# Kernel tuning notes

Measured on AMD Instinct MI355X. Metric: run time of the kernel, lower is better.

## Reference

```python
import jax, jax.numpy as jnp
import numpy as np

B, S, D, C, K, V = 128, 512, 300, 300, 3, 30000  # batch, seq, embed=hidden, capsule, categories, vocab
PAD_INDEX = 0
SQUASH_EPS = 1e-8
MASK_NEG = -1e9


def squash(x, axis=-1):
    # v * (|v|^2 / (1+|v|^2)) / |v|
    sq = jnp.sum(x * x, axis=axis, keepdims=True)
    return (sq / (1.0 + sq)) * x / jnp.sqrt(sq + SQUASH_EPS)


def setup_inputs() -> dict:
    key = jax.random.key(0)
    ks = jax.random.split(key, 11)
    return {
        "sentence": jax.random.randint(ks[0], (B, S), 0, V),
        "aspect": jax.random.randint(ks[1], (B,), 0, V),
        "category_alpha": jax.random.uniform(ks[2], (B, S), dtype=jnp.float32),
        "embed": jax.random.normal(ks[3], (V, D), dtype=jnp.float32) * 0.02,
        "W_s": jax.random.normal(ks[4], (D, C), dtype=jnp.float32) * 0.02,
        "b_s": jnp.zeros((C,), dtype=jnp.float32),
        "W_a": jax.random.normal(ks[5], (D, C), dtype=jnp.float32) * 0.02,
        "b_a": jnp.zeros((C,), dtype=jnp.float32),
        "W_att": jax.random.normal(ks[6], (C, C), dtype=jnp.float32) * 0.02,
        "guide_capsule": jax.random.normal(ks[7], (K, C), dtype=jnp.float32) * 0.02,
        "guide_weight": jax.random.normal(ks[8], (C, C), dtype=jnp.float32) * 0.02,
        "scale": jnp.asarray(5.0, dtype=jnp.float32),
    }


def reference(sentence, aspect, category_alpha, embed, W_s, b_s, W_a, b_a,
              W_att, guide_capsule, guide_weight, scale):
    mask = sentence != PAD_INDEX                      # [B,S]
    emb = embed[sentence]                             # [B,S,D]
    asp = embed[aspect]                               # [B,D]

    # element_wise_mul (vectorized): per-token alpha weighting
    caml = emb * category_alpha[..., None]            # [B,S,D]
    cavl = jnp.sum(caml, axis=1)                      # [B,D] (unused in non-Cav path)
    del cavl

    # _sentence_encode stand-in (abstract in source): alpha-weighted embeddings
    sent_enc = caml                                   # [B,S,hidden=D]

    primary = squash(sent_enc @ W_s + b_s)            # [B,S,C]
    aspect_capsule = squash(asp @ W_a + b_a)          # [B,C]

    # bilinear attention weights with padding mask, softmax over sequence
    scores = jnp.einsum('bsc,cd,bd->bs', primary, W_att, aspect_capsule)
    scores = jnp.where(mask, scores, MASK_NEG)
    norm_weight = jax.nn.softmax(scores, axis=-1)     # [B,S]

    # capsule-guided routing
    guide = squash(guide_capsule)                     # [K,C]
    gm = jnp.einsum('bsc,cd,kd->bsk', primary, guide_weight, guide)
    gm = jax.nn.softmax(gm, axis=-1) * norm_weight[..., None] * scale
    category_capsule = squash(jnp.einsum('bsk,bsc->bkc', gm, primary))  # [B,K,C]

    return jnp.sqrt(jnp.sum(category_capsule * category_capsule, axis=-1))  # [B,K]
```

## Files before the change

### kernel.cpp

```cpp
#include <hip/hip_runtime.h>

#define NV 30000
#define NB 128
#define NS 512
#define ND 300
#define NC 300
#define CP 304
#define KP 320
#define MASK_NEG -1e9f
#define SQ_EPS 1e-8f

typedef __attribute__((ext_vector_type(4))) float f32x4;
typedef __attribute__((ext_vector_type(8))) __bf16 bf16x8;

__device__ __forceinline__ unsigned int f2bfu(float x){
  unsigned int u = __float_as_uint(x);
  u += 0x7FFFu + ((u >> 16) & 1u);
  return u >> 16;
}
__device__ __forceinline__ unsigned short f2bf(float x){ return (unsigned short)f2bfu(x); }

__device__ __forceinline__ int swzk(int row, int k){
  return (k & ~0x38) | (((((k >> 3) & 7) ^ (row & 7)) & 7) << 3);
}

__device__ __forceinline__ float bsum512(float v, float* red, int tid){
  red[tid] = v; __syncthreads();
  float s = 0.f;
  if (tid < 64){
    s = red[tid]+red[tid+64]+red[tid+128]+red[tid+192]
      + red[tid+256]+red[tid+320]+red[tid+384]+red[tid+448];
    #pragma unroll
    for (int off = 32; off > 0; off >>= 1) s += __shfl_xor(s, off);
    if (tid == 0) red[0] = s;
  }
  __syncthreads();
  s = red[0];
  __syncthreads();
  return s;
}

__device__ __forceinline__ float bmax512(float v, float* red, int tid){
  red[tid] = v; __syncthreads();
  float s = MASK_NEG;
  if (tid < 64){
    s = red[tid];
    #pragma unroll
    for (int o = 64; o < 512; o += 64) s = fmaxf(s, red[tid+o]);
    #pragma unroll
    for (int off = 32; off > 0; off >>= 1) s = fmaxf(s, __shfl_xor(s, off));
    if (tid == 0) red[0] = s;
  }
  __syncthreads();
  s = red[0];
  __syncthreads();
  return s;
}

__global__ __launch_bounds__(512) void kA(
    const float* __restrict__ Ws, const float* __restrict__ Wa,
    const float* __restrict__ ba, const int* __restrict__ aspect,
    const float* __restrict__ embed, const float* __restrict__ gcap,
    const float* __restrict__ Gw, const float* __restrict__ bs,
    unsigned short* __restrict__ WTC, float* __restrict__ ZG,
    float* __restrict__ Z2P, float* __restrict__ TG)
{
  __shared__ __align__(16) char shm[55296];
  int bid = blockIdx.x, tid = threadIdx.x;
  int lane = tid & 63, wid = tid >> 6;
  if (bid < 25){
    float (*t)[65] = (float(*)[65])shm;
    int kt = bid / 5, nt = bid - kt*5;
    #pragma unroll
    for (int i = 0; i < 8; i++){
      int idx = i*512 + tid;
      int r = idx >> 6, c = idx & 63;
      int gk = kt*64 + r, gn = nt*64 + c;
      t[r][c] = (gk < ND && gn < NC) ? Ws[gk*NC + gn] : 0.f;
    }
    __syncthreads();
    #pragma unroll
    for (int i = 0; i < 8; i++){
      int idx = i*512 + tid;
      int n = idx >> 6, k = idx & 63;
      int row = nt*64 + n, gk = kt*64 + k;
      WTC[(size_t)row*KP + swzk(row, gk)] = f2bf(t[k][n]);
    }
    if (bid < 24){
      for (int r = 0; r < 8; r++){
        int row = 320 + bid*8 + r;
        if (tid < KP) WTC[(size_t)row*KP + tid] = 0;
      }
    }
  } else if (bid < 45){
    unsigned short (*ATF)[72] = (unsigned short (*)[72])shm;
    unsigned short (*ldbz)[72] = (unsigned short (*)[72])(shm + 128*144);
    int* toksh = (int*)(shm + 144*144);
    int zb = bid - 25;
    int nc0 = zb * 16;
    if (tid < 128) toksh[tid] = aspect[tid];
    __syncthreads();
    f32x4 accz = {0.f,0.f,0.f,0.f};
    for (int s = 0; s < 5; s++){
      int k0 = s*64;
      #pragma unroll
      for (int i = 0; i < 4; i++){
        int idx = i*512 + tid;
        int row = idx >> 4, q = idx & 15;
        int gk = k0 + 4*q;
        float4 v = {0.f,0.f,0.f,0.f};
        if (gk < ND) v = *(const float4*)(embed + (size_t)toksh[row]*ND + gk);
        uint2 pk; pk.x = f2bfu(v.x)|(f2bfu(v.y)<<16); pk.y = f2bfu(v.z)|(f2bfu(v.w)<<16);
        *(uint2*)(&ATF[row][4*q]) = pk;
      }
      if (tid < 256){
        int dl = tid >> 2, qq = tid & 3;
        int d = k0 + dl, c = nc0 + 4*qq;
        float4 v = {0.f,0.f,0.f,0.f};
        if (d < ND && c < NC) v = *(const float4*)(Wa + (size_t)d*NC + c);
        ldbz[4*qq+0][dl] = f2bf(v.x);
        ldbz[4*qq+1][dl] = f2bf(v.y);
        ldbz[4*qq+2][dl] = f2bf(v.z);
        ldbz[4*qq+3][dl] = f2bf(v.w);
      }
      __syncthreads();
      #pragma unroll
      for (int kk = 0; kk < 64; kk += 32){
        int kl = kk + (lane >> 4)*8;
        bf16x8 a = *(const bf16x8*)(&ATF[wid*16 + (lane & 15)][kl]);
        bf16x8 b = *(const bf16x8*)(&ldbz[lane & 15][kl]);
        accz = __builtin_amdgcn_mfma_f32_16x16x32_bf16(a, b, accz, 0, 0, 0);
      }
      __syncthreads();
    }
    int zc = nc0 + (lane & 15);
    float bav = (zc < NC) ? ba[zc] : 0.f;
    #pragma unroll
    for (int j = 0; j < 4; j++){
      int row = wid*16 + ((lane >> 4) << 2) + j;
      float zv = (zc < NC) ? (accz[j] + bav) : 0.f;
      ZG[(size_t)row*KP + zc] = zv;
      float p = zv*zv;
      #pragma unroll
      for (int off = 1; off < 16; off <<= 1) p += __shfl_xor(p, off);
      if ((lane & 15) == 0) Z2P[zb*128 + row] = p;
    }
  } else {
    unsigned short (*Ag)[328] = (unsigned short (*)[328])shm;
    unsigned short (*ldbg)[328] = (unsigned short (*)[328])(shm + 16*656);
    float* red = (float*)(shm + 80*656);
    int gb = bid - 45, c0 = gb*64;
    for (int k = 0; k < 3; k++){
      float g = (tid < NC) ? gcap[k*NC + tid] : 0.f;
      float sq = bsum512(g*g, red, tid);
      float ssv = (sq/(1.f+sq))/sqrtf(sq + SQ_EPS);
      if (tid < 328) Ag[k][tid] = (tid < NC) ? f2bf(g*ssv) : (unsigned short)0;
    }
    for (int r = 3; r < 16; r++) if (tid < 328) Ag[r][tid] = 0;
    #pragma unroll
    for (int i = 0; i < 10; i++){
      int idx = i*512 + tid;
      int cl = idx / 80, q = idx - cl*80;
      float4 v = {0.f,0.f,0.f,0.f};
      if (c0 + cl < NC && q < 75) v = *(const float4*)(Gw + (size_t)(c0+cl)*NC + 4*q);
      uint2 pk; pk.x = f2bfu(v.x)|(f2bfu(v.y)<<16); pk.y = f2bfu(v.z)|(f2bfu(v.w)<<16);
      *(uint2*)(&ldbg[cl][4*q]) = pk;
    }
    __syncthreads();
    if (wid < 4){
      f32x4 acc = {0.f,0.f,0.f,0.f};
      #pragma unroll
      for (int kk = 0; kk < KP; kk += 32){
        int kidx = kk + (lane >> 4)*8;
        bf16x8 a = *(const bf16x8*)(&Ag[lane & 15][kidx]);
        bf16x8 b = *(const bf16x8*)(&ldbg[wid*16 + (lane & 15)][kidx]);
        acc = __builtin_amdgcn_mfma_f32_16x16x32_bf16(a, b, acc, 0, 0, 0);
      }
      #pragma unroll
      for (int j = 0; j < 4; j++){
        int r = ((lane >> 4) << 2) + j;
        if (r < 3) TG[(size_t)(128 + r)*KP + c0 + wid*16 + (lane & 15)] = acc[j];
      }
    }
    if (gb == 0 && tid < KP) TG[(size_t)131*KP + tid] = (tid < NC) ? bs[tid] : 0.f;
  }
}

__global__ __launch_bounds__(512) void kB(
    const float* __restrict__ ZG, const float* __restrict__ Z2P,
    const float* __restrict__ Watt, float* __restrict__ TG)
{
  __shared__ unsigned short ATF[128][72];
  __shared__ unsigned short ldbt[16][72];
  __shared__ float ssb[128];
  int tid = threadIdx.x, lane = tid & 63, wid = tid >> 6;
  int c0 = blockIdx.x * 16;
  if (tid < 128){
    float s = 0.f;
    #pragma unroll
    for (int i = 0; i < 20; i++) s += Z2P[i*128 + tid];
    ssb[tid] = (s/(1.f+s))/sqrtf(s + SQ_EPS);
  }
  __syncthreads();
  f32x4 acct = {0.f,0.f,0.f,0.f};
  for (int s = 0; s < 5; s++){
    int k0 = s*64;
    #pragma unroll
    for (int i = 0; i < 4; i++){
      int idx = i*512 + tid;
      int row = idx >> 4, q = idx & 15;
      float4 v = *(const float4*)(ZG + (size_t)row*KP + k0 + 4*q);
      float sv = ssb[row];
      uint2 pk; pk.x = f2bfu(v.x*sv)|(f2bfu(v.y*sv)<<16); pk.y = f2bfu(v.z*sv)|(f2bfu(v.w*sv)<<16);
      *(uint2*)(&ATF[row][4*q]) = pk;
    }
    if (tid < 256){
      int cl = tid >> 4, q = tid & 15;
      int gc = k0 + 4*q;
      float4 v = {0.f,0.f,0.f,0.f};
      if (c0 + cl < NC && gc < NC) v = *(const float4*)(Watt + (size_t)(c0+cl)*NC + gc);
      uint2 pk; pk.x = f2bfu(v.x)|(f2bfu(v.y)<<16); pk.y = f2bfu(v.z)|(f2bfu(v.w)<<16);
      *(uint2*)(&ldbt[cl][4*q]) = pk;
    }
    __syncthreads();
    #pragma unroll
    for (int kk = 0; kk < 64; kk += 32){
      int kl = kk + (lane >> 4)*8;
      bf16x8 a = *(const bf16x8*)(&ATF[wid*16 + (lane & 15)][kl]);
      bf16x8 b = *(const bf16x8*)(&ldbt[lane & 15][kl]);
      acct = __builtin_amdgcn_mfma_f32_16x16x32_bf16(a, b, acct, 0, 0, 0);
    }
    __syncthreads();
  }
  int cc = c0 + (lane & 15);
  #pragma unroll
  for (int j = 0; j < 4; j++){
    int row = wid*16 + ((lane >> 4) << 2) + j;
    TG[(size_t)row*KP + cc] = acct[j];
  }
}

__global__ __launch_bounds__(512) void kC(
    const float* __restrict__ TG, const float* __restrict__ Ws,
    const float* __restrict__ bs,
    unsigned short* __restrict__ WTC, float* __restrict__ BC)
{
  __shared__ unsigned short ATF[144][72];
  __shared__ unsigned short ldbw[16][72];
  int tid = threadIdx.x, lane = tid & 63, wid = tid >> 6;
  int wb = blockIdx.x;
  int d0 = wb*16;
  f32x4 aw0 = {0.f,0.f,0.f,0.f}, aw8 = {0.f,0.f,0.f,0.f};
  for (int s = 0; s < 5; s++){
    int k0 = s*64;
    #pragma unroll
    for (int i = 0; i < 5; i++){
      int idx = i*512 + tid;
      if (idx < 2304){
        int row = idx >> 4, q = idx & 15;
        float4 v = {0.f,0.f,0.f,0.f};
        if (row < 132) v = *(const float4*)(TG + (size_t)row*KP + k0 + 4*q);
        uint2 pk; pk.x = f2bfu(v.x)|(f2bfu(v.y)<<16); pk.y = f2bfu(v.z)|(f2bfu(v.w)<<16);
        *(uint2*)(&ATF[row][4*q]) = pk;
      }
    }
    if (tid < 256){
      int dl = tid >> 4, q = tid & 15;
      int gc = k0 + 4*q;
      float4 v = {0.f,0.f,0.f,0.f};
      if (gc < NC){
        if (wb < 20){ if (d0 + dl < ND) v = *(const float4*)(Ws + (size_t)(d0+dl)*NC + gc); }
        else if (dl == 0) v = *(const float4*)(bs + gc);
      }
      uint2 pk; pk.x = f2bfu(v.x)|(f2bfu(v.y)<<16); pk.y = f2bfu(v.z)|(f2bfu(v.w)<<16);
      *(uint2*)(&ldbw[dl][4*q]) = pk;
    }
    __syncthreads();
    #pragma unroll
    for (int kk = 0; kk < 64; kk += 32){
      int kl = kk + (lane >> 4)*8;
      bf16x8 b = *(const bf16x8*)(&ldbw[lane & 15][kl]);
      bf16x8 a = *(const bf16x8*)(&ATF[wid*16 + (lane & 15)][kl]);
      aw0 = __builtin_amdgcn_mfma_f32_16x16x32_bf16(a, b, aw0, 0, 0, 0);
      bf16x8 a8 = *(const bf16x8*)(&ATF[128 + (lane & 15)][kl]);
      aw8 = __builtin_amdgcn_mfma_f32_16x16x32_bf16(a8, b, aw8, 0, 0, 0);
    }
    __syncthreads();
  }
  int gd = lane & 15;
  #pragma unroll
  for (int j = 0; j < 4; j++){
    int row = wid*16 + ((lane >> 4) << 2) + j;
    if (wb < 20){
      int col = d0 + gd;
      if (col < ND) WTC[(size_t)(320 + row)*KP + swzk(320 + row, col)] = f2bf(aw0[j]);
    } else if (gd == 0) BC[row] = aw0[j];
    if (wid == 0){
      int row8 = 128 + ((lane >> 4) << 2) + j;
      if (row8 < 132){
        if (wb < 20){
          int col = d0 + gd;
          if (col < ND) WTC[(size_t)(320 + row8)*KP + swzk(320 + row8, col)] = f2bf(aw8[j]);
        } else if (gd == 0) BC[row8] = aw8[j];
      }
    }
  }
}

#define LDK 72
__global__ __launch_bounds__(512, 4) void k1f(
    const float* __restrict__ embed, const unsigned short* __restrict__ WTC,
    float* __restrict__ EtT, float* __restrict__ ETS)
{
  __shared__ unsigned short lds_a[64*LDK];
  __shared__ unsigned short lds_b[512*64];
  __shared__ float e2part[3][64];
  int tid = threadIdx.x, lane = tid & 63, wid = tid >> 6;
  int wrow = wid >> 2, wcol = wid & 3;
  int rowbase = blockIdx.x * 64;
  f32x4 acc[2][8];
  f32x4 zero = {0.f,0.f,0.f,0.f};
  #pragma unroll
  for (int m = 0; m < 2; m++)
    #pragma unroll
    for (int n = 0; n < 8; n++) acc[m][n] = zero;

  float4 pa[2];
  auto loadA = [&](int k0){
    #pragma unroll
    for (int r = 0; r < 2; r++){
      int id = r*512 + tid;
      int row = id >> 4, k4 = (id & 15) << 2;
      int grow = rowbase + row, gk = k0 + k4;
      float4 v = {0.f,0.f,0.f,0.f};
      if (grow < NV && gk < ND) v = *(const float4*)(embed + (size_t)grow*ND + gk);
      pa[r] = v;
    }
  };
  auto writeA = [&](){
    #pragma unroll
    for (int r = 0; r < 2; r++){
      int id = r*512 + tid;
      int row = id >> 4, k4 = (id & 15) << 2;
      uint2 pk;
      pk.x = f2bfu(pa[r].x) | (f2bfu(pa[r].y) << 16);
      pk.y = f2bfu(pa[r].z) | (f2bfu(pa[r].w) << 16);
      *(uint2*)(lds_a + row*LDK + k4) = pk;
    }
  };
  auto stageB = [&](int k0){
    #pragma unroll
    for (int r = 0; r < 8; r++){
      int id = r*512 + tid;
      const unsigned short* gsrc = WTC + (size_t)(id >> 3)*KP + k0 + (id & 7)*8;
      __builtin_amdgcn_global_load_lds(
        (const __attribute__((address_space(1))) unsigned int*)gsrc,
        (__attribute__((address_space(3))) unsigned int*)((char*)lds_b + id*16),
        16, 0, 0);
    }
  };

  loadA(0);
  writeA();
  stageB(0);
  loadA(64);
  __syncthreads();
  for (int step = 0; step < 5; step++){
    #pragma unroll
    for (int kk = 0; kk < 64; kk += 32){
      int kidx = kk + (lane >> 4)*8;
      bf16x8 af[2];
      #pragma unroll
      for (int m = 0; m < 2; m++)
        af[m] = *(const bf16x8*)(lds_a + (wrow*32 + (lane & 15) + m*16)*LDK + kidx);
      #pragma unroll
      for (int n = 0; n < 8; n++){
        int jrow = wcol*128 + n*16 + (lane & 15);
        int ch = ((kidx >> 3) & 7) ^ (jrow & 7);
        bf16x8 bv = *(const bf16x8*)((const char*)lds_b + jrow*128 + ch*16);
        #pragma unroll
        for (int m = 0; m < 2; m++)
          acc[m][n] = __builtin_amdgcn_mfma_f32_16x16x32_bf16(af[m], bv, acc[m][n], 0, 0, 0);
      }
    }
    __syncthreads();
    if (step < 4){
      stageB((step+1)*64);
      writeA();
      if (step < 3) loadA((step+2)*64);
      __syncthreads();
    }
  }

  float* etile = (float*)lds_b;
  float* stile = (float*)((char*)lds_b + 32768);
  int rloc = wrow*32 + ((lane >> 4) << 2);
  #pragma unroll
  for (int m = 0; m < 2; m++)
    #pragma unroll
    for (int n = 0; n < 8; n++){
      int col = wcol*128 + n*16 + (lane & 15);
      #pragma unroll
      for (int j = 0; j < 4; j++){
        int rl = rloc + m*16 + j;
        if (col >= 320 && col < 448)      etile[rl*128 + (col - 320)] = acc[m][n][j];
        else if (col >= 448 && col < 452) stile[rl*8 + (col - 448)] = acc[m][n][j];
      }
    }
  #pragma unroll
  for (int m = 0; m < 2; m++)
    #pragma unroll
    for (int j = 0; j < 4; j++){
      float p = 0.f;
      #pragma unroll
      for (int n = 0; n < 8; n++)
        if (wcol*128 + n*16 < 320){ float t = acc[m][n][j]; p += t*t; }
      #pragma unroll
      for (int off = 1; off < 16; off <<= 1) p += __shfl_xor(p, off);
      if ((lane & 15) == 0 && wcol < 3) e2part[wcol][rloc + m*16 + j] = p;
    }
  __syncthreads();
  if (tid < 64){
    stile[tid*8 + 4] = e2part[0][tid] + e2part[1][tid] + e2part[2][tid];
    stile[tid*8 + 5] = 0.f; stile[tid*8 + 6] = 0.f; stile[tid*8 + 7] = 0.f;
  }
  __syncthreads();
  int nrow = NV - rowbase; if (nrow > 64) nrow = 64;
  float4* edst = (float4*)(EtT + (size_t)rowbase*128);
  const float4* esrc = (const float4*)etile;
  int e4 = nrow*32;
  for (int i = tid; i < e4; i += 512) edst[i] = esrc[i];
  float4* sdst = (float4*)(ETS + (size_t)rowbase*8);
  const float4* ssrc = (const float4*)stile;
  int s4 = nrow*2;
  for (int i = tid; i < s4; i += 512) sdst[i] = ssrc[i];
}

__global__ __launch_bounds__(512) void k45a(
    const int* __restrict__ sentence, const float* __restrict__ alpha,
    const float* __restrict__ scale_p, const float* __restrict__ embed,
    const float* __restrict__ EtT, const float* __restrict__ ETS,
    const float* __restrict__ BC, float* __restrict__ SBB, float* __restrict__ PRT)
{
  int bid = blockIdx.x;
  int b = bid >> 1, hb = bid & 1;
  int tid = threadIdx.x, lane = tid & 63, w = tid >> 6;
  __shared__ float red[512];
  __shared__ float cfs[NS*3];
  __shared__ int toksh[NS];
  __shared__ float cap8[8][3][CP];

  int idx = (b << 9) + tid;
  int tok = sentence[idx];
  float al = alpha[idx];
  toksh[tid] = tok;
  float et = EtT[(size_t)tok*128 + b];
  float4 eg = *(const float4*)(ETS + (size_t)tok*8);
  float e2 = ETS[(size_t)tok*8 + 4];
  float bst = BC[b];
  float bsg0 = BC[128], bsg1 = BC[129], bsg2 = BC[130], bs2 = BC[131];

  float sq = al*al*e2 + 2.f*al*eg.w + bs2;
  float ssv = (sq/(1.f+sq))/sqrtf(sq + SQ_EPS);
  float scv = (tok != 0) ? ssv*(al*et + bst) : MASK_NEG;
  float u0 = ssv*(al*eg.x + bsg0);
  float u1 = ssv*(al*eg.y + bsg1);
  float u2 = ssv*(al*eg.z + bsg2);

  float m = bmax512(scv, red, tid);
  float e = expf(scv - m);
  float Z = bsum512(e, red, tid);
  float nw = e / Z;
  float mk = fmaxf(u0, fmaxf(u1, u2));
  float e0 = expf(u0-mk), e1 = expf(u1-mk), e2k = expf(u2-mk);
  float wf = nw * scale_p[0] / (e0+e1+e2k);
  float w0 = e0*wf, w1 = e1*wf, w2 = e2k*wf;
  float ca = ssv * al;
  cfs[tid*3+0] = w0*ca; cfs[tid*3+1] = w1*ca; cfs[tid*3+2] = w2*ca;
  float sb0 = bsum512(w0*ssv, red, tid);
  float sb1 = bsum512(w1*ssv, red, tid);
  float sb2 = bsum512(w2*ssv, red, tid);
  if (hb == 0 && tid == 0){ SBB[b*3+0] = sb0; SBB[b*3+1] = sb1; SBB[b*3+2] = sb2; }
  __syncthreads();

  f32x4 A0 = {0.f,0.f,0.f,0.f}, A1 = A0, A2 = A0, R0 = A0, R1 = A0, R2 = A0;
  int c0 = lane << 2;
  int c1 = 256 + (lane << 2);
  bool rem = lane < 11;
  int base = (hb << 8) + (w << 5);
  #pragma unroll 4
  for (int i = 0; i < 32; i++){
    int s = base + i;
    int t = toksh[s];
    const float* er = embed + (size_t)t*ND;
    float4 y = *(const float4*)(er + c0);
    float cf0 = cfs[s*3+0], cf1 = cfs[s*3+1], cf2 = cfs[s*3+2];
    f32x4 yv = {y.x, y.y, y.z, y.w};
    A0 += cf0*yv; A1 += cf1*yv; A2 += cf2*yv;
    if (rem){
      float4 y2 = *(const float4*)(er + c1);
      f32x4 y2v = {y2.x, y2.y, y2.z, y2.w};
      R0 += cf0*y2v; R1 += cf1*y2v; R2 += cf2*y2v;
    }
  }
  *(f32x4*)&cap8[w][0][c0] = A0;
  *(f32x4*)&cap8[w][1][c0] = A1;
  *(f32x4*)&cap8[w][2][c0] = A2;
  if (rem){
    *(f32x4*)&cap8[w][0][c1] = R0;
    *(f32x4*)&cap8[w][1][c1] = R1;
    *(f32x4*)&cap8[w][2][c1] = R2;
  }
  __syncthreads();
  for (int p = tid; p < 3*CP; p += 512){
    int k = p / CP, c = p - k*CP;
    float v = 0.f;
    if (c < 300){
      #pragma unroll
      for (int w8 = 0; w8 < 8; w8++) v += cap8[w8][k][c];
    }
    PRT[((size_t)bid*3 + k)*CP + c] = v;
  }
}

__global__ __launch_bounds__(512) void k45b(
    const float* __restrict__ PRT, const float* __restrict__ SBB,
    const float* __restrict__ bs, const float* __restrict__ Ws,
    float* __restrict__ out)
{
  int b = blockIdx.x, tid = threadIdx.x;
  __shared__ float Qs[3][CP];
  __shared__ float red[512];
  for (int p = tid; p < 3*CP; p += 512){
    int k = p / CP, c = p - k*CP;
    float v = 0.f;
    if (c < 300)
      v = PRT[((size_t)(2*b)*3 + k)*CP + c] + PRT[((size_t)(2*b+1)*3 + k)*CP + c];
    Qs[k][c] = v;
  }
  __syncthreads();
  float v0 = 0.f, v1 = 0.f, v2 = 0.f;
  if (tid < NC){
    float a0=0.f,a1=0.f,a2=0.f,b0=0.f,b1=0.f,b2=0.f;
    for (int d = 0; d < 300; d += 2){
      float wA = Ws[d*NC + tid], wB = Ws[(d+1)*NC + tid];
      a0 += wA*Qs[0][d]; b0 += wB*Qs[0][d+1];
      a1 += wA*Qs[1][d]; b1 += wB*Qs[1][d+1];
      a2 += wA*Qs[2][d]; b2 += wB*Qs[2][d+1];
    }
    float bc = bs[tid];
    v0 = a0+b0 + SBB[b*3+0]*bc;
    v1 = a1+b1 + SBB[b*3+1]*bc;
    v2 = a2+b2 + SBB[b*3+2]*bc;
  }
  float s0 = bsum512(v0*v0, red, tid);
  float s1 = bsum512(v1*v1, red, tid);
  float s2 = bsum512(v2*v2, red, tid);
  if (tid == 0){
    out[b*3+0] = (s0/(1.f+s0))*sqrtf(s0)/sqrtf(s0 + SQ_EPS);
    out[b*3+1] = (s1/(1.f+s1))*sqrtf(s1)/sqrtf(s1 + SQ_EPS);
    out[b*3+2] = (s2/(1.f+s2))*sqrtf(s2)/sqrtf(s2 + SQ_EPS);
  }
}

extern "C" void kernel_launch(void* const* d_in, const int* in_sizes, int n_in,
                              void* d_out, int out_size, void* d_ws, size_t ws_size,
                              hipStream_t stream)
{
  (void)in_sizes; (void)n_in; (void)out_size; (void)ws_size;
  const int*   sentence = (const int*)d_in[0];
  const int*   aspect   = (const int*)d_in[1];
  const float* alpha    = (const float*)d_in[2];
  const float* embed    = (const float*)d_in[3];
  const float* Ws       = (const float*)d_in[4];
  const float* bs       = (const float*)d_in[5];
  const float* Wa       = (const float*)d_in[6];
  const float* ba       = (const float*)d_in[7];
  const float* Watt     = (const float*)d_in[8];
  const float* gcap     = (const float*)d_in[9];
  const float* gw       = (const float*)d_in[10];
  const float* scale    = (const float*)d_in[11];
  float* out = (float*)d_out;

  char* w = (char*)d_ws;
  auto alloc = [&](size_t bytes)->char*{
    char* p = w; w += (bytes + 255) & ~(size_t)255; return p;
  };
  unsigned short* WTC = (unsigned short*)alloc((size_t)512*KP*2);
  float* ZG  = (float*)alloc((size_t)128*KP*4);
  float* Z2P = (float*)alloc((size_t)20*128*4);
  float* TG  = (float*)alloc((size_t)132*KP*4);
  float* BC  = (float*)alloc(136*4);
  float* ETT = (float*)alloc((size_t)NV*128*4);
  float* ETS = (float*)alloc((size_t)NV*8*4);
  float* SBB = (float*)alloc(NB*3*4);
  float* PRT = (float*)alloc((size_t)256*3*CP*4);

  kA<<<50, 512, 0, stream>>>(Ws, Wa, ba, aspect, embed, gcap, gw, bs, WTC, ZG, Z2P, TG);
  kB<<<20, 512, 0, stream>>>(ZG, Z2P, Watt, TG);
  kC<<<21, 512, 0, stream>>>(TG, Ws, bs, WTC, BC);
  k1f<<<(NV + 63)/64, 512, 0, stream>>>(embed, WTC, ETT, ETS);
  k45a<<<256, 512, 0, stream>>>(sentence, alpha, scale, embed, ETT, ETS, BC, SBB, PRT);
  k45b<<<NB, 512, 0, stream>>>(PRT, SBB, bs, Ws, out);
}
```

Baseline: 93.27 us.

## Fuse kB and kC into one kernel, recomputing the full TG tile per block

Merges the two small GEMM kernels kB and kC into a single kernel, kBC. Each of the 21 blocks now computes the entire 128x300 TG product from Watt into LDS instead of reading it back from global memory. This removes one kernel launch and the global round-trip of TG between launches. The cost is redundant compute in every block, a large LDS footprint that can limit occupancy, and 19 accumulator vectors per thread that raise register pressure.

```diff
diff --git a/kernel.cpp b/kernel.cpp
--- a/kernel.cpp
+++ b/kernel.cpp
@@ -186,15 +186,20 @@
   }
 }
 
-__global__ __launch_bounds__(512) void kB(
+__global__ __launch_bounds__(512) void kBC(
     const float* __restrict__ ZG, const float* __restrict__ Z2P,
-    const float* __restrict__ Watt, float* __restrict__ TG)
+    const float* __restrict__ Watt, const float* __restrict__ TG,
+    const float* __restrict__ Ws, const float* __restrict__ bs,
+    unsigned short* __restrict__ WTC, float* __restrict__ BC)
 {
+  __shared__ unsigned short TL[144][328];
   __shared__ unsigned short ATF[128][72];
-  __shared__ unsigned short ldbt[16][72];
+  __shared__ unsigned short LB[304][72];
   __shared__ float ssb[128];
   int tid = threadIdx.x, lane = tid & 63, wid = tid >> 6;
-  int c0 = blockIdx.x * 16;
+  int wb = blockIdx.x;
+
+  for (int i = tid; i < 144*328/8; i += 512) ((uint4*)TL)[i] = (uint4){0u,0u,0u,0u};
   if (tid < 128){
     float s = 0.f;
     #pragma unroll
@@ -202,7 +207,10 @@
     ssb[tid] = (s/(1.f+s))/sqrtf(s + SQ_EPS);
   }
   __syncthreads();
-  f32x4 acct = {0.f,0.f,0.f,0.f};
+
+  f32x4 acc[19];
+  #pragma unroll
+  for (int ch = 0; ch < 19; ch++) acc[ch] = (f32x4){0.f,0.f,0.f,0.f};
   for (int s = 0; s < 5; s++){
     int k0 = s*64;
     #pragma unroll
@@ -214,56 +222,50 @@
       uint2 pk; pk.x = f2bfu(v.x*sv)|(f2bfu(v.y*sv)<<16); pk.y = f2bfu(v.z*sv)|(f2bfu(v.w*sv)<<16);
       *(uint2*)(&ATF[row][4*q]) = pk;
     }
-    if (tid < 256){
-      int cl = tid >> 4, q = tid & 15;
-      int gc = k0 + 4*q;
-      float4 v = {0.f,0.f,0.f,0.f};
-      if (c0 + cl < NC && gc < NC) v = *(const float4*)(Watt + (size_t)(c0+cl)*NC + gc);
-      uint2 pk; pk.x = f2bfu(v.x)|(f2bfu(v.y)<<16); pk.y = f2bfu(v.z)|(f2bfu(v.w)<<16);
-      *(uint2*)(&ldbt[cl][4*q]) = pk;
+    #pragma unroll
+    for (int i = 0; i < 10; i++){
+      int idx = i*512 + tid;
+      if (idx < 4864){
+        int cl = idx >> 4, q = idx & 15;
+        int gc = k0 + 4*q;
+        float4 v = {0.f,0.f,0.f,0.f};
+        if (cl < NC && gc < NC) v = *(const float4*)(Watt + (size_t)cl*NC + gc);
+        uint2 pk; pk.x = f2bfu(v.x)|(f2bfu(v.y)<<16); pk.y = f2bfu(v.z)|(f2bfu(v.w)<<16);
+        *(uint2*)(&LB[cl][4*q]) = pk;
+      }
     }
     __syncthreads();
     #pragma unroll
     for (int kk = 0; kk < 64; kk += 32){
       int kl = kk + (lane >> 4)*8;
       bf16x8 a = *(const bf16x8*)(&ATF[wid*16 + (lane & 15)][kl]);
-      bf16x8 b = *(const bf16x8*)(&ldbt[lane & 15][kl]);
-      acct = __builtin_amdgcn_mfma_f32_16x16x32_bf16(a, b, acct, 0, 0, 0);
-    }
-    __syncthreads();
-  }
-  int cc = c0 + (lane & 15);
+      #pragma unroll
+      for (int ch = 0; ch < 19; ch++){
+        bf16x8 b = *(const bf16x8*)(&LB[ch*16 + (lane & 15)][kl]);
+        acc[ch] = __builtin_amdgcn_mfma_f32_16x16x32_bf16(a, b, acc[ch], 0, 0, 0);
+      }
+    }
+    __syncthreads();
+  }
   #pragma unroll
-  for (int j = 0; j < 4; j++){
-    int row = wid*16 + ((lane >> 4) << 2) + j;
-    TG[(size_t)row*KP + cc] = acct[j];
-  }
-}
-
-__global__ __launch_bounds__(512) void kC(
-    const float* __restrict__ TG, const float* __restrict__ Ws,
-    const float* __restrict__ bs,
-    unsigned short* __restrict__ WTC, float* __restrict__ BC)
-{
-  __shared__ unsigned short ATF[144][72];
-  __shared__ unsigned short ldbw[16][72];
-  int tid = threadIdx.x, lane = tid & 63, wid = tid >> 6;
-  int wb = blockIdx.x;
+  for (int ch = 0; ch < 19; ch++)
+    #pragma unroll
+    for (int j = 0; j < 4; j++){
+      int row = wid*16 + ((lane >> 4) << 2) + j;
+      int col = ch*16 + (lane & 15);
+      TL[row][col] = f2bf(acc[ch][j]);
+    }
+  for (int idx = tid; idx < 4*KP; idx += 512){
+    int r = idx / KP, c = idx - r*KP;
+    TL[128 + r][c] = f2bf(TG[(size_t)(128 + r)*KP + c]);
+  }
+  __syncthreads();
+
+  unsigned short (*ldbw)[72] = (unsigned short (*)[72])ATF;
   int d0 = wb*16;
   f32x4 aw0 = {0.f,0.f,0.f,0.f}, aw8 = {0.f,0.f,0.f,0.f};
   for (int s = 0; s < 5; s++){
     int k0 = s*64;
-    #pragma unroll
-    for (int i = 0; i < 5; i++){
-      int idx = i*512 + tid;
-      if (idx < 2304){
-        int row = idx >> 4, q = idx & 15;
-        float4 v = {0.f,0.f,0.f,0.f};
-        if (row < 132) v = *(const float4*)(TG + (size_t)row*KP + k0 + 4*q);
-        uint2 pk; pk.x = f2bfu(v.x)|(f2bfu(v.y)<<16); pk.y = f2bfu(v.z)|(f2bfu(v.w)<<16);
-        *(uint2*)(&ATF[row][4*q]) = pk;
-      }
-    }
     if (tid < 256){
       int dl = tid >> 4, q = tid & 15;
       int gc = k0 + 4*q;
@@ -280,9 +282,9 @@
     for (int kk = 0; kk < 64; kk += 32){
       int kl = kk + (lane >> 4)*8;
       bf16x8 b = *(const bf16x8*)(&ldbw[lane & 15][kl]);
-      bf16x8 a = *(const bf16x8*)(&ATF[wid*16 + (lane & 15)][kl]);
+      bf16x8 a = *(const bf16x8*)(&TL[wid*16 + (lane & 15)][k0 + kl]);
       aw0 = __builtin_amdgcn_mfma_f32_16x16x32_bf16(a, b, aw0, 0, 0, 0);
-      bf16x8 a8 = *(const bf16x8*)(&ATF[128 + (lane & 15)][kl]);
+      bf16x8 a8 = *(const bf16x8*)(&TL[128 + (lane & 15)][k0 + kl]);
       aw8 = __builtin_amdgcn_mfma_f32_16x16x32_bf16(a8, b, aw8, 0, 0, 0);
     }
     __syncthreads();
@@ -597,8 +599,7 @@
   float* PRT = (float*)alloc((size_t)256*3*CP*4);
 
   kA<<<50, 512, 0, stream>>>(Ws, Wa, ba, aspect, embed, gcap, gw, bs, WTC, ZG, Z2P, TG);
-  kB<<<20, 512, 0, stream>>>(ZG, Z2P, Watt, TG);
-  kC<<<21, 512, 0, stream>>>(TG, Ws, bs, WTC, BC);
+  kBC<<<21, 512, 0, stream>>>(ZG, Z2P, Watt, TG, Ws, bs, WTC, BC);
   k1f<<<(NV + 63)/64, 512, 0, stream>>>(embed, WTC, ETT, ETS);
   k45a<<<256, 512, 0, stream>>>(sentence, alpha, scale, embed, ETT, ETS, BC, SBB, PRT);
   k45b<<<NB, 512, 0, stream>>>(PRT, SBB, bs, Ws, out);
```

Measured after the change: 99.89 us. 1.07x slower.

## Fuse k45a and k45b into one kernel per batch row

Applied to the files above, without the earlier changes.

Merges the two-block-per-batch gather/accumulate kernel with the follow-up projection and squash kernel, so each block handles one full batch row and applies the Ws projection directly from shared memory. This drops one kernel launch and the PRT/SBB global round trip. In exchange the grid halves from 256 to 128 blocks, and each wave now walks 64 tokens instead of 32, which lowers parallelism in the gather phase.

```diff
diff --git a/kernel.cpp b/kernel.cpp
--- a/kernel.cpp
+++ b/kernel.cpp
@@ -436,19 +436,20 @@
   for (int i = tid; i < s4; i += 512) sdst[i] = ssrc[i];
 }
 
-__global__ __launch_bounds__(512) void k45a(
+__global__ __launch_bounds__(512) void k45(
     const int* __restrict__ sentence, const float* __restrict__ alpha,
     const float* __restrict__ scale_p, const float* __restrict__ embed,
     const float* __restrict__ EtT, const float* __restrict__ ETS,
-    const float* __restrict__ BC, float* __restrict__ SBB, float* __restrict__ PRT)
+    const float* __restrict__ BC, const float* __restrict__ bs,
+    const float* __restrict__ Ws, float* __restrict__ out)
 {
-  int bid = blockIdx.x;
-  int b = bid >> 1, hb = bid & 1;
+  int b = blockIdx.x;
   int tid = threadIdx.x, lane = tid & 63, w = tid >> 6;
   __shared__ float red[512];
   __shared__ float cfs[NS*3];
   __shared__ int toksh[NS];
   __shared__ float cap8[8][3][CP];
+  __shared__ float Qs[3][CP];
 
   int idx = (b << 9) + tid;
   int tok = sentence[idx];
@@ -480,16 +481,15 @@
   float sb0 = bsum512(w0*ssv, red, tid);
   float sb1 = bsum512(w1*ssv, red, tid);
   float sb2 = bsum512(w2*ssv, red, tid);
-  if (hb == 0 && tid == 0){ SBB[b*3+0] = sb0; SBB[b*3+1] = sb1; SBB[b*3+2] = sb2; }
   __syncthreads();
 
   f32x4 A0 = {0.f,0.f,0.f,0.f}, A1 = A0, A2 = A0, R0 = A0, R1 = A0, R2 = A0;
   int c0 = lane << 2;
   int c1 = 256 + (lane << 2);
   bool rem = lane < 11;
-  int base = (hb << 8) + (w << 5);
+  int base = w << 6;
   #pragma unroll 4
-  for (int i = 0; i < 32; i++){
+  for (int i = 0; i < 64; i++){
     int s = base + i;
     int t = toksh[s];
     const float* er = embed + (size_t)t*ND;
@@ -519,23 +519,6 @@
       #pragma unroll
       for (int w8 = 0; w8 < 8; w8++) v += cap8[w8][k][c];
     }
-    PRT[((size_t)bid*3 + k)*CP + c] = v;
-  }
-}
-
-__global__ __launch_bounds__(512) void k45b(
-    const float* __restrict__ PRT, const float* __restrict__ SBB,
-    const float* __restrict__ bs, const float* __restrict__ Ws,
-    float* __restrict__ out)
-{
-  int b = blockIdx.x, tid = threadIdx.x;
-  __shared__ float Qs[3][CP];
-  __shared__ float red[512];
-  for (int p = tid; p < 3*CP; p += 512){
-    int k = p / CP, c = p - k*CP;
-    float v = 0.f;
-    if (c < 300)
-      v = PRT[((size_t)(2*b)*3 + k)*CP + c] + PRT[((size_t)(2*b+1)*3 + k)*CP + c];
     Qs[k][c] = v;
   }
   __syncthreads();
@@ -549,9 +532,9 @@
       a2 += wA*Qs[2][d]; b2 += wB*Qs[2][d+1];
     }
     float bc = bs[tid];
-    v0 = a0+b0 + SBB[b*3+0]*bc;
-    v1 = a1+b1 + SBB[b*3+1]*bc;
-    v2 = a2+b2 + SBB[b*3+2]*bc;
+    v0 = a0+b0 + sb0*bc;
+    v1 = a1+b1 + sb1*bc;
+    v2 = a2+b2 + sb2*bc;
   }
   float s0 = bsum512(v0*v0, red, tid);
   float s1 = bsum512(v1*v1, red, tid);
@@ -593,13 +576,10 @@
   float* BC  = (float*)alloc(136*4);
   float* ETT = (float*)alloc((size_t)NV*128*4);
   float* ETS = (float*)alloc((size_t)NV*8*4);
-  float* SBB = (float*)alloc(NB*3*4);
-  float* PRT = (float*)alloc((size_t)256*3*CP*4);
 
   kA<<<50, 512, 0, stream>>>(Ws, Wa, ba, aspect, embed, gcap, gw, bs, WTC, ZG, Z2P, TG);
   kB<<<20, 512, 0, stream>>>(ZG, Z2P, Watt, TG);
   kC<<<21, 512, 0, stream>>>(TG, Ws, bs, WTC, BC);
   k1f<<<(NV + 63)/64, 512, 0, stream>>>(embed, WTC, ETT, ETS);
-  k45a<<<256, 512, 0, stream>>>(sentence, alpha, scale, embed, ETT, ETS, BC, SBB, PRT);
-  k45b<<<NB, 512, 0, stream>>>(PRT, SBB, bs, Ws, out);
-}
+  k45<<<NB, 512, 0, stream>>>(sentence, alpha, scale, embed, ETT, ETS, BC, bs, Ws, out);
+}
```

New measurement: 101.0 us. 8.3% more time.
